# Optimization experiments

Measured on AMD Instinct MI355X. Metric: run time of the kernel, lower is better.

## Reference

```python
import jax, jax.numpy as jnp
import numpy as np

EPS = 1e-12


def sage_pool_conv(x, src, dst, W_pool, b_pool, W_self, W_neigh, b, num_nodes):
    """DGL SAGEConv with aggregator_type='pool':
    h_neigh[v] = max_{u in N(v)} relu(x[u] @ W_pool + b_pool)
    out[v] = x[v] @ W_self + h_neigh[v] @ W_neigh + b
    Zero-in-degree nodes get h_neigh = 0 (DGL fills max over empty set with 0).
    """
    m = jax.nn.relu(x[src] @ W_pool + b_pool)            # [E, F] gathered + transformed
    agg = jax.ops.segment_max(m, dst, num_segments=num_nodes)  # [N, F], -inf where no neighbors
    agg = jnp.where(jnp.isneginf(agg), 0.0, agg)
    return x @ W_self + agg @ W_neigh + b


def l2norm_relu(h):
    # F.normalize(h, p=2, dim=1, eps=1e-12) then relu
    n = jnp.maximum(jnp.linalg.norm(h, axis=1, keepdims=True), EPS)
    return jax.nn.relu(h / n)


def setup_inputs() -> dict:
    key = jax.random.key(0)
    N, E = 50000, 1600000
    IN, HID, OUT = 128, 128, 128
    ks = jax.random.split(key, 16)
    s = 0.05
    return {
        "x": jax.random.normal(ks[0], (N, IN), dtype=jnp.float32),
        "src": jax.random.randint(ks[1], (E,), 0, N, dtype=jnp.int32),
        "dst": jax.random.randint(ks[2], (E,), 0, N, dtype=jnp.int32),
        "W_pool1": jax.random.normal(ks[3], (IN, IN), dtype=jnp.float32) * s,
        "b_pool1": jnp.zeros((IN,), dtype=jnp.float32),
        "W_self1": jax.random.normal(ks[4], (IN, HID), dtype=jnp.float32) * s,
        "W_neigh1": jax.random.normal(ks[5], (IN, HID), dtype=jnp.float32) * s,
        "b1": jnp.zeros((HID,), dtype=jnp.float32),
        "W_pool2": jax.random.normal(ks[6], (HID, HID), dtype=jnp.float32) * s,
        "b_pool2": jnp.zeros((HID,), dtype=jnp.float32),
        "W_self2": jax.random.normal(ks[7], (HID, OUT), dtype=jnp.float32) * s,
        "W_neigh2": jax.random.normal(ks[8], (HID, OUT), dtype=jnp.float32) * s,
        "b2": jnp.zeros((OUT,), dtype=jnp.float32),
    }


def reference(x, src, dst, W_pool1, b_pool1, W_self1, W_neigh1, b1,
              W_pool2, b_pool2, W_self2, W_neigh2, b2):
    N = x.shape[0]
    h = sage_pool_conv(x, src, dst, W_pool1, b_pool1, W_self1, W_neigh1, b1, N)
    h = l2norm_relu(h)
    # dropout_1 is re-assigned in the original forward but never applied -> no dropout
    h = sage_pool_conv(h, src, dst, W_pool2, b_pool2, W_self2, W_neigh2, b2, N)
    h = l2norm_relu(h)
    return h
```

## Files before the change

### kernel.cpp

```cpp
#include <hip/hip_runtime.h>
#include <hip/hip_bf16.h>

#define NF 128

typedef __attribute__((ext_vector_type(8))) short bf8;
typedef __attribute__((ext_vector_type(4))) float f4;
typedef unsigned short u16x8 __attribute__((ext_vector_type(8)));

static __device__ __forceinline__ unsigned short f2bf(float f) {
  unsigned u = __builtin_bit_cast(unsigned, f);
  u = u + 0x7FFF + ((u >> 16) & 1);
  return (unsigned short)(u >> 16);
}

static __device__ __forceinline__ uint4 pkmax4(uint4 a, uint4 b) {
  u16x8 x = __builtin_bit_cast(u16x8, a);
  u16x8 y = __builtin_bit_cast(u16x8, b);
  u16x8 m = __builtin_elementwise_max(x, y);
  return __builtin_bit_cast(uint4, m);
}

static __device__ __forceinline__ uint4 shflxor4(uint4 a, int m) {
  uint4 r;
  r.x = (unsigned)__shfl_xor((int)a.x, m, 64);
  r.y = (unsigned)__shfl_xor((int)a.y, m, 64);
  r.z = (unsigned)__shfl_xor((int)a.z, m, 64);
  r.w = (unsigned)__shfl_xor((int)a.w, m, 64);
  return r;
}


__global__ void k_convX(const float* __restrict__ A, unsigned short* __restrict__ B,
                        long long nelem, int* __restrict__ bcnt, int nb) {
  long long i = (long long)(blockIdx.x * blockDim.x + threadIdx.x) * 8;
  if (blockIdx.x == 0 && (int)threadIdx.x < nb) bcnt[threadIdx.x] = 0;
  if (i + 8 > nelem) return;
  float4 a = *(const float4*)(A + i);
  float4 b = *(const float4*)(A + i + 4);
  uint4 o;
  o.x = f2bf(a.x) | ((unsigned)f2bf(a.y) << 16);
  o.y = f2bf(a.z) | ((unsigned)f2bf(a.w) << 16);
  o.z = f2bf(b.x) | ((unsigned)f2bf(b.y) << 16);
  o.w = f2bf(b.z) | ((unsigned)f2bf(b.w) << 16);
  *(uint4*)(B + i) = o;
}


__global__ void k_packW(const float* W0, const float* W1, const float* W2,
                        const float* W3, const float* W4, const float* W5,
                        unsigned short* __restrict__ out) {
  int gid = blockIdx.x * blockDim.x + threadIdx.x;
  int m = gid >> 11;
  int u = gid & 2047;
  if (m >= 6) return;
  const float* W = (m == 0) ? W0 : (m == 1) ? W1 : (m == 2) ? W2
                 : (m == 3) ? W3 : (m == 4) ? W4 : W5;
  int l = u & 63, c = u >> 6;
  int kk = c & 3, t = c >> 2;
  int kb = kk * 32 + ((l >> 4) << 3);
  int n = t * 16 + (l & 15);
  unsigned short* o = out + (size_t)m * 2048 * 8 + (size_t)u * 8;
  #pragma unroll
  for (int j = 0; j < 8; ++j) o[j] = f2bf(W[(size_t)(kb + j) * NF + n]);
}


#define TILE_B 8192

__global__ __launch_bounds__(256) void k_bhist(const int* __restrict__ dst,
                                               int* __restrict__ bcnt, int E) {
  __shared__ int h[256];
  int tid = threadIdx.x;
  h[tid] = 0;
  __syncthreads();
  int t0 = blockIdx.x * TILE_B;
  int tend = min(E, t0 + TILE_B);
  for (int i = t0 + tid; i < tend; i += 256) atomicAdd(&h[dst[i] >> 8], 1);
  __syncthreads();
  if (h[tid] > 0) atomicAdd(&bcnt[tid], h[tid]);
}

__global__ __launch_bounds__(256) void k_bscan(const int* __restrict__ bcnt,
                                               int* __restrict__ boff,
                                               int* __restrict__ cursors,
                                               int* __restrict__ off,
                                               int nb, int N, int E) {
  __shared__ int sc[256];
  int tid = threadIdx.x;
  int v = (tid < nb) ? bcnt[tid] : 0;
  sc[tid] = v;
  __syncthreads();
  for (int d = 1; d < 256; d <<= 1) {
    int t = (tid >= d) ? sc[tid - d] : 0;
    __syncthreads();
    sc[tid] += t;
    __syncthreads();
  }
  if (tid < nb) {
    boff[tid + 1] = sc[tid];
    cursors[tid] = sc[tid] - v;
  }
  if (tid == 0) { boff[0] = 0; off[N] = E; }
}

__global__ __launch_bounds__(256) void k_binB(const int* __restrict__ src,
                                              const int* __restrict__ dst,
                                              int* __restrict__ cursors,
                                              unsigned* __restrict__ tmp, int E) {
  __shared__ int h[256], sc[256], gb[256], lc[256];
  __shared__ unsigned sorted[TILE_B];
  int tid = threadIdx.x;
  int t0 = blockIdx.x * TILE_B;
  int tcnt = min(E - t0, TILE_B);
  if (tcnt <= 0) return;
  h[tid] = 0;
  __syncthreads();
  for (int i = tid; i < tcnt; i += 256) atomicAdd(&h[dst[t0 + i] >> 8], 1);
  __syncthreads();
  int v = h[tid];
  sc[tid] = v;
  __syncthreads();
  for (int d = 1; d < 256; d <<= 1) {
    int t = (tid >= d) ? sc[tid - d] : 0;
    __syncthreads();
    sc[tid] += t;
    __syncthreads();
  }
  lc[tid] = 0;
  gb[tid] = (v > 0) ? atomicAdd(&cursors[tid], v) : 0;
  __syncthreads();
  for (int i = tid; i < tcnt; i += 256) {
    int d = dst[t0 + i];
    unsigned s = (unsigned)src[t0 + i];
    int b = d >> 8;
    int p = (sc[b] - h[b]) + atomicAdd(&lc[b], 1);
    sorted[p] = ((unsigned)b << 24) | (s << 8) | (unsigned)(d & 255);
  }
  __syncthreads();
  for (int i = tid; i < tcnt; i += 256) {
    unsigned ev = sorted[i];
    int b = ev >> 24;
    tmp[gb[b] + (i - (sc[b] - h[b]))] = ev & 0xFFFFFFu;
  }
}

#define CSR_CAP 15360

__global__ __launch_bounds__(256) void k_binC(const unsigned* __restrict__ tmp,
                                              const int* __restrict__ boff,
                                              int* __restrict__ off,
                                              unsigned short* __restrict__ esrc, int N) {
  __shared__ int lh[256], ls[256], lcur[256];
  __shared__ int csr[CSR_CAP];
  int tid = threadIdx.x;
  int b = blockIdx.x;
  int base = b << 8;
  int beg = boff[b], end = boff[b + 1];
  int cnt = end - beg;
  lh[tid] = 0;
  __syncthreads();
  for (int i = beg + tid; i < end; i += 256) atomicAdd(&lh[tmp[i] & 255], 1);
  __syncthreads();
  int v = lh[tid];
  ls[tid] = v;
  __syncthreads();
  for (int d = 1; d < 256; d <<= 1) {
    int t = (tid >= d) ? ls[tid - d] : 0;
    __syncthreads();
    ls[tid] += t;
    __syncthreads();
  }
  int excl = ls[tid] - v;
  if (base + tid < N) off[base + tid] = beg + excl;
  lcur[tid] = 0;
  __syncthreads();
  if (cnt <= CSR_CAP) {
    for (int i = beg + tid; i < end; i += 256) {
      unsigned e = tmp[i];
      int dl = (int)(e & 255);
      int p = (ls[dl] - lh[dl]) + atomicAdd(&lcur[dl], 1);
      csr[p] = (int)(e >> 8);
    }
    __syncthreads();
    for (int i = tid; i < cnt; i += 256) esrc[beg + i] = (unsigned short)csr[i];
  } else {
    for (int i = beg + tid; i < end; i += 256) {
      unsigned e = tmp[i];
      int dl = (int)(e & 255);
      int p = (ls[dl] - lh[dl]) + atomicAdd(&lcur[dl], 1);
      esrc[beg + p] = (unsigned short)(e >> 8);
    }
  }
}


__global__ __launch_bounds__(256) void k_gemm_pool(
    const unsigned short* __restrict__ A, const unsigned short* __restrict__ P,
    const float* __restrict__ bias, unsigned short* __restrict__ Yout, int M) {
  __shared__ __align__(16) char smem[32768];
  int tid = threadIdx.x, w = tid >> 6, lane = tid & 63;
  int r0 = lane & 15, g = lane >> 4;
  int base = blockIdx.x * 64;
  int arow = min(base + w * 16 + r0, M - 1);

  {
    uint4* S = (uint4*)smem;
    const uint4* Pv = (const uint4*)P;
    for (int t = tid; t < 2048; t += 256) S[t] = Pv[t];
  }
  __syncthreads();

  f4 acc[8];
  #pragma unroll
  for (int t = 0; t < 8; ++t) acc[t] = (f4){0.f, 0.f, 0.f, 0.f};

  const bf8* Ar = (const bf8*)(A + (size_t)arow * NF);
  const bf8* Wl = (const bf8*)smem;
  #pragma unroll
  for (int kk = 0; kk < 4; ++kk) {
    bf8 a = Ar[kk * 4 + g];
    #pragma unroll
    for (int t = 0; t < 8; ++t) {
      bf8 b = Wl[(t * 4 + kk) * 64 + lane];
      acc[t] = __builtin_amdgcn_mfma_f32_16x16x32_bf16(a, b, acc[t], 0, 0, 0);
    }
  }

  float bb[8];
  #pragma unroll
  for (int t = 0; t < 8; ++t) bb[t] = bias[t * 16 + r0];

  __syncthreads();
  unsigned short* So = (unsigned short*)smem;
  #pragma unroll
  for (int i = 0; i < 4; ++i)
    #pragma unroll
    for (int t = 0; t < 8; ++t)
      So[(w * 16 + g * 4 + i) * NF + t * 16 + r0] = f2bf(fmaxf(acc[t][i] + bb[t], 0.f));
  __syncthreads();
  int maxrows = min(64, M - base);
  uint4* Og = (uint4*)(Yout + (size_t)base * NF);
  const uint4* Sv = (const uint4*)smem;
  int maxc = maxrows * 16;
  for (int c = tid; c < 1024; c += 256)
    if (c < maxc) Og[c] = Sv[c];
}


__global__ __launch_bounds__(256) void k_gather_max(
    const unsigned short* __restrict__ Y, const int* __restrict__ off,
    const unsigned short* __restrict__ esrc, unsigned short* __restrict__ AGG, int N) {
  int w = (blockIdx.x * 256 + threadIdx.x) >> 6;
  int lane = threadIdx.x & 63;
  if (w >= N) return;
  int r0 = lane & 15, g = lane >> 4;
  int s = __builtin_amdgcn_readfirstlane(off[w]);
  int e = __builtin_amdgcn_readfirstlane(off[w + 1]);
  uint4 am[4];
  #pragma unroll
  for (int j = 0; j < 4; ++j) am[j] = (uint4){0u, 0u, 0u, 0u};
  for (int b0 = s; b0 < e; b0 += 64) {
    int cnt = min(64, e - b0);
    int idxv = (int)esrc[b0 + min(lane, cnt - 1)];
    for (int i = 0; i < cnt; i += 16) {
      #pragma unroll
      for (int j = 0; j < 4; ++j) {
        int eo = min(i + j * 4 + g, cnt - 1);
        int u = __shfl(idxv, eo, 64);
        uint4 v = *((const uint4*)(Y + (size_t)u * NF) + r0);
        am[j] = pkmax4(am[j], v);
      }
    }
  }
  uint4 a01 = pkmax4(am[0], am[1]);
  uint4 a23 = pkmax4(am[2], am[3]);
  uint4 a = pkmax4(a01, a23);
  a = pkmax4(a, shflxor4(a, 16));
  a = pkmax4(a, shflxor4(a, 32));
  if (g == 0) *(uint4*)(AGG + (size_t)w * NF + r0 * 8) = a;
}


template <int OUT_MODE>
__global__ __launch_bounds__(256) void k_gemm_dual(
    const unsigned short* __restrict__ A0, const unsigned short* __restrict__ P0,
    const unsigned short* __restrict__ A1, const unsigned short* __restrict__ P1,
    const float* __restrict__ bias, void* __restrict__ Cout, int M) {
  __shared__ __align__(16) char smem[65536];
  int tid = threadIdx.x, w = tid >> 6, lane = tid & 63;
  int r0 = lane & 15, g = lane >> 4;
  int base = blockIdx.x * 64;
  int arow = min(base + w * 16 + r0, M - 1);

  {
    uint4* S = (uint4*)smem;
    const uint4* Pv0 = (const uint4*)P0;
    const uint4* Pv1 = (const uint4*)P1;
    for (int t = tid; t < 2048; t += 256) S[t] = Pv0[t];
    for (int t = tid; t < 2048; t += 256) S[2048 + t] = Pv1[t];
  }
  __syncthreads();

  f4 acc[8];
  #pragma unroll
  for (int t = 0; t < 8; ++t) acc[t] = (f4){0.f, 0.f, 0.f, 0.f};

  #pragma unroll
  for (int mat = 0; mat < 2; ++mat) {
    const unsigned short* A = (mat == 0) ? A0 : A1;
    const bf8* Ar = (const bf8*)(A + (size_t)arow * NF);
    const bf8* Wl = (const bf8*)smem + (size_t)mat * 2048;
    #pragma unroll
    for (int kk = 0; kk < 4; ++kk) {
      bf8 a = Ar[kk * 4 + g];
      #pragma unroll
      for (int t = 0; t < 8; ++t) {
        bf8 b = Wl[(t * 4 + kk) * 64 + lane];
        acc[t] = __builtin_amdgcn_mfma_f32_16x16x32_bf16(a, b, acc[t], 0, 0, 0);
      }
    }
  }

  float bb[8];
  #pragma unroll
  for (int t = 0; t < 8; ++t) bb[t] = bias[t * 16 + r0];

  float val[8][4];
  #pragma unroll
  for (int t = 0; t < 8; ++t)
    #pragma unroll
    for (int i = 0; i < 4; ++i) val[t][i] = acc[t][i] + bb[t];

  float ss[4] = {0.f, 0.f, 0.f, 0.f};
  #pragma unroll
  for (int i = 0; i < 4; ++i)
    #pragma unroll
    for (int t = 0; t < 8; ++t) ss[i] += val[t][i] * val[t][i];
  #pragma unroll
  for (int d = 1; d < 16; d <<= 1)
    #pragma unroll
    for (int i = 0; i < 4; ++i) ss[i] += __shfl_xor(ss[i], d, 64);
  float inv[4];
  #pragma unroll
  for (int i = 0; i < 4; ++i) inv[i] = 1.f / fmaxf(sqrtf(ss[i]), 1e-12f);

  __syncthreads();
  int maxrows = min(64, M - base);

  if (OUT_MODE == 2) {
    float* So = (float*)smem;
    #pragma unroll
    for (int i = 0; i < 4; ++i)
      #pragma unroll
      for (int t = 0; t < 8; ++t)
        So[(w * 16 + g * 4 + i) * NF + t * 16 + r0] = fmaxf(val[t][i] * inv[i], 0.f);
    __syncthreads();
    uint4* Og = (uint4*)((float*)Cout + (size_t)base * NF);
    const uint4* Sv = (const uint4*)smem;
    int maxc = maxrows * 32;
    for (int c = tid; c < 2048; c += 256)
      if (c < maxc) Og[c] = Sv[c];
  } else {
    unsigned short* So = (unsigned short*)smem;
    #pragma unroll
    for (int i = 0; i < 4; ++i)
      #pragma unroll
      for (int t = 0; t < 8; ++t)
        So[(w * 16 + g * 4 + i) * NF + t * 16 + r0] = f2bf(fmaxf(val[t][i] * inv[i], 0.f));
    __syncthreads();
    uint4* Og = (uint4*)((unsigned short*)Cout + (size_t)base * NF);
    const uint4* Sv = (const uint4*)smem;
    int maxc = maxrows * 16;
    for (int c = tid; c < 1024; c += 256)
      if (c < maxc) Og[c] = Sv[c];
  }
}


extern "C" void kernel_launch(void* const* d_in, const int* in_sizes, int n_in,
                              void* d_out, int out_size, void* d_ws, size_t ws_size,
                              hipStream_t stream) {
  const float* x   = (const float*)d_in[0];
  const int*   src = (const int*)d_in[1];
  const int*   dst = (const int*)d_in[2];
  const float* Wp1 = (const float*)d_in[3];
  const float* bp1 = (const float*)d_in[4];
  const float* Ws1 = (const float*)d_in[5];
  const float* Wn1 = (const float*)d_in[6];
  const float* b1  = (const float*)d_in[7];
  const float* Wp2 = (const float*)d_in[8];
  const float* bp2 = (const float*)d_in[9];
  const float* Ws2 = (const float*)d_in[10];
  const float* Wn2 = (const float*)d_in[11];
  const float* b2  = (const float*)d_in[12];
  float* out = (float*)d_out;

  const int N = in_sizes[0] / NF;
  const int E = in_sizes[1];
  const int NB = (N + 255) >> 8;

  char* ws = (char*)d_ws;
  auto carve = [&](size_t bytes) { char* p = ws; ws += (bytes + 255) & ~(size_t)255; return p; };
  unsigned short* Xb    = (unsigned short*)carve((size_t)N * NF * 2);
  unsigned short* Yb    = (unsigned short*)carve((size_t)N * NF * 2);
  unsigned short* AGGb  = (unsigned short*)carve((size_t)N * NF * 2);
  unsigned short* Hb    = (unsigned short*)carve((size_t)N * NF * 2);
  unsigned short* Wpack = (unsigned short*)carve((size_t)6 * NF * NF * 2);
  int* off     = (int*)carve((size_t)(N + 1) * 4);
  int* bcnt    = (int*)carve((size_t)NB * 4);
  int* boff    = (int*)carve((size_t)(NB + 1) * 4);
  int* cursors = (int*)carve((size_t)NB * 4);
  unsigned* tmp = (unsigned*)carve((size_t)E * 4);
  unsigned short* esrc = (unsigned short*)carve((size_t)E * 2);

  unsigned short* Pp1 = Wpack + 0 * NF * NF;
  unsigned short* Ps1 = Wpack + 1 * NF * NF;
  unsigned short* Pn1 = Wpack + 2 * NF * NF;
  unsigned short* Pp2 = Wpack + 3 * NF * NF;
  unsigned short* Ps2 = Wpack + 4 * NF * NF;
  unsigned short* Pn2 = Wpack + 5 * NF * NF;

  const long long nelX = (long long)N * NF;
  const int gConv = (int)((nelX / 8 + 255) / 256);
  const int gPack = (6 * 2048 + 255) / 256;
  const int gTile = (E + TILE_B - 1) / TILE_B;
  const int gG    = (N + 63) / 64;
  const int gRW   = (N + 3) / 4;

  k_convX<<<gConv, 256, 0, stream>>>(x, Xb, nelX, bcnt, NB);
  k_packW<<<gPack, 256, 0, stream>>>(Wp1, Ws1, Wn1, Wp2, Ws2, Wn2, Wpack);

  k_bhist<<<gTile, 256, 0, stream>>>(dst, bcnt, E);
  k_bscan<<<1, 256, 0, stream>>>(bcnt, boff, cursors, off, NB, N, E);
  k_binB<<<gTile, 256, 0, stream>>>(src, dst, cursors, tmp, E);
  k_binC<<<NB, 256, 0, stream>>>(tmp, boff, off, esrc, N);

  k_gemm_pool<<<gG, 256, 0, stream>>>(Xb, Pp1, bp1, Yb, N);
  k_gather_max<<<gRW, 256, 0, stream>>>(Yb, off, esrc, AGGb, N);
  k_gemm_dual<1><<<gG, 256, 0, stream>>>(Xb, Ps1, AGGb, Pn1, b1, Hb, N);

  k_gemm_pool<<<gG, 256, 0, stream>>>(Hb, Pp2, bp2, Yb, N);
  k_gather_max<<<gRW, 256, 0, stream>>>(Yb, off, esrc, AGGb, N);
  k_gemm_dual<2><<<gG, 256, 0, stream>>>(Hb, Ps2, AGGb, Pn2, b2, out, N);
}
```

Baseline: 296.0 us.

## Merge prep kernels, use persistent GEMM blocks, deepen gather loads

Folds the bf16 conversion of x, the weight packing and the destination histogram into one prep kernel, with a memset zeroing the bucket counts, so fewer kernels are launched. Replaces the per-64-row GEMM kernels with one persistent template that uses 512-thread blocks and a fixed grid. Each wave loops over 16-row tiles and stages its output in a private shared-memory area, so weight loads are amortized and block-wide barriers are avoided. The gather-max kernel now issues 8 independent row loads before reducing them, to keep more memory requests in flight at the cost of more registers.

```diff
diff --git a/kernel.cpp b/kernel.cpp
--- a/kernel.cpp
+++ b/kernel.cpp
@@ -30,55 +30,53 @@
 }
 
 
-__global__ void k_convX(const float* __restrict__ A, unsigned short* __restrict__ B,
-                        long long nelem, int* __restrict__ bcnt, int nb) {
-  long long i = (long long)(blockIdx.x * blockDim.x + threadIdx.x) * 8;
-  if (blockIdx.x == 0 && (int)threadIdx.x < nb) bcnt[threadIdx.x] = 0;
-  if (i + 8 > nelem) return;
-  float4 a = *(const float4*)(A + i);
-  float4 b = *(const float4*)(A + i + 4);
-  uint4 o;
-  o.x = f2bf(a.x) | ((unsigned)f2bf(a.y) << 16);
-  o.y = f2bf(a.z) | ((unsigned)f2bf(a.w) << 16);
-  o.z = f2bf(b.x) | ((unsigned)f2bf(b.y) << 16);
-  o.w = f2bf(b.z) | ((unsigned)f2bf(b.w) << 16);
-  *(uint4*)(B + i) = o;
-}
-
-
-__global__ void k_packW(const float* W0, const float* W1, const float* W2,
-                        const float* W3, const float* W4, const float* W5,
-                        unsigned short* __restrict__ out) {
-  int gid = blockIdx.x * blockDim.x + threadIdx.x;
-  int m = gid >> 11;
-  int u = gid & 2047;
-  if (m >= 6) return;
-  const float* W = (m == 0) ? W0 : (m == 1) ? W1 : (m == 2) ? W2
-                 : (m == 3) ? W3 : (m == 4) ? W4 : W5;
-  int l = u & 63, c = u >> 6;
-  int kk = c & 3, t = c >> 2;
-  int kb = kk * 32 + ((l >> 4) << 3);
-  int n = t * 16 + (l & 15);
-  unsigned short* o = out + (size_t)m * 2048 * 8 + (size_t)u * 8;
-  #pragma unroll
-  for (int j = 0; j < 8; ++j) o[j] = f2bf(W[(size_t)(kb + j) * NF + n]);
-}
-
-
 #define TILE_B 8192
 
-__global__ __launch_bounds__(256) void k_bhist(const int* __restrict__ dst,
-                                               int* __restrict__ bcnt, int E) {
+__global__ __launch_bounds__(256) void k_prep(
+    const float* __restrict__ x, unsigned short* __restrict__ Xb, long long nelX,
+    const int* __restrict__ dst, int* __restrict__ bcnt, int E, int gTile,
+    const float* W0, const float* W1, const float* W2,
+    const float* W3, const float* W4, const float* W5,
+    unsigned short* __restrict__ Wpack) {
   __shared__ int h[256];
-  int tid = threadIdx.x;
-  h[tid] = 0;
-  __syncthreads();
-  int t0 = blockIdx.x * TILE_B;
-  int tend = min(E, t0 + TILE_B);
-  for (int i = t0 + tid; i < tend; i += 256) atomicAdd(&h[dst[i] >> 8], 1);
-  __syncthreads();
-  if (h[tid] > 0) atomicAdd(&bcnt[tid], h[tid]);
-}
+  int b = blockIdx.x, tid = threadIdx.x;
+
+  long long i = ((long long)b * 256 + tid) * 8;
+  if (i + 8 <= nelX) {
+    float4 a = *(const float4*)(x + i);
+    float4 c = *(const float4*)(x + i + 4);
+    uint4 o;
+    o.x = f2bf(a.x) | ((unsigned)f2bf(a.y) << 16);
+    o.y = f2bf(a.z) | ((unsigned)f2bf(a.w) << 16);
+    o.z = f2bf(c.x) | ((unsigned)f2bf(c.y) << 16);
+    o.w = f2bf(c.z) | ((unsigned)f2bf(c.w) << 16);
+    *(uint4*)(Xb + i) = o;
+  }
+
+  if (b < gTile) {
+    h[tid] = 0;
+    __syncthreads();
+    int t0 = b * TILE_B;
+    int tend = min(E, t0 + TILE_B);
+    for (int k = t0 + tid; k < tend; k += 256) atomicAdd(&h[dst[k] >> 8], 1);
+    __syncthreads();
+    if (h[tid] > 0) atomicAdd(&bcnt[tid], h[tid]);
+  } else if (b < gTile + 48) {
+    int gid = (b - gTile) * 256 + tid;
+    int m = gid >> 11;
+    int u = gid & 2047;
+    const float* W = (m == 0) ? W0 : (m == 1) ? W1 : (m == 2) ? W2
+                   : (m == 3) ? W3 : (m == 4) ? W4 : W5;
+    int l = u & 63, c = u >> 6;
+    int kk = c & 3, t = c >> 2;
+    int kb = kk * 32 + ((l >> 4) << 3);
+    int n = t * 16 + (l & 15);
+    unsigned short* o = Wpack + (size_t)m * 2048 * 8 + (size_t)u * 8;
+    #pragma unroll
+    for (int j = 0; j < 8; ++j) o[j] = f2bf(W[(size_t)(kb + j) * NF + n]);
+  }
+}
+
 
 __global__ __launch_bounds__(256) void k_bscan(const int* __restrict__ bcnt,
                                                int* __restrict__ boff,
@@ -194,35 +192,23 @@
 }
 
 
-__global__ __launch_bounds__(256) void k_gemm_pool(
-    const unsigned short* __restrict__ A, const unsigned short* __restrict__ P,
-    const float* __restrict__ bias, unsigned short* __restrict__ Yout, int M) {
-  __shared__ __align__(16) char smem[32768];
+template <int NMAT, int OUT_MODE>
+__global__ __launch_bounds__(512) void k_gemm_p(
+    const unsigned short* __restrict__ A0, const unsigned short* __restrict__ P0,
+    const unsigned short* __restrict__ A1, const unsigned short* __restrict__ P1,
+    const float* __restrict__ bias, void* __restrict__ Cout, int M) {
+  constexpr int STG = (OUT_MODE == 2) ? 8192 : 4096;
+  __shared__ __align__(16) char smem[NMAT * 32768 + 8 * STG];
   int tid = threadIdx.x, w = tid >> 6, lane = tid & 63;
   int r0 = lane & 15, g = lane >> 4;
-  int base = blockIdx.x * 64;
-  int arow = min(base + w * 16 + r0, M - 1);
 
   {
     uint4* S = (uint4*)smem;
-    const uint4* Pv = (const uint4*)P;
-    for (int t = tid; t < 2048; t += 256) S[t] = Pv[t];
-  }
-  __syncthreads();
-
-  f4 acc[8];
-  #pragma unroll
-  for (int t = 0; t < 8; ++t) acc[t] = (f4){0.f, 0.f, 0.f, 0.f};
-
-  const bf8* Ar = (const bf8*)(A + (size_t)arow * NF);
-  const bf8* Wl = (const bf8*)smem;
-  #pragma unroll
-  for (int kk = 0; kk < 4; ++kk) {
-    bf8 a = Ar[kk * 4 + g];
-    #pragma unroll
-    for (int t = 0; t < 8; ++t) {
-      bf8 b = Wl[(t * 4 + kk) * 64 + lane];
-      acc[t] = __builtin_amdgcn_mfma_f32_16x16x32_bf16(a, b, acc[t], 0, 0, 0);
+    const uint4* Pv0 = (const uint4*)P0;
+    for (int t = tid; t < 2048; t += 512) S[t] = Pv0[t];
+    if (NMAT == 2) {
+      const uint4* Pv1 = (const uint4*)P1;
+      for (int t = tid; t < 2048; t += 512) S[2048 + t] = Pv1[t];
     }
   }
 
@@ -231,19 +217,89 @@
   for (int t = 0; t < 8; ++t) bb[t] = bias[t * 16 + r0];
 
   __syncthreads();
-  unsigned short* So = (unsigned short*)smem;
-  #pragma unroll
-  for (int i = 0; i < 4; ++i)
+  const bf8* Wl = (const bf8*)smem;
+  char* myst = smem + NMAT * 32768 + w * STG;
+
+  int T = (M + 15) >> 4;
+  int stride = gridDim.x * 8;
+  for (int t0i = blockIdx.x * 8 + w; t0i < T; t0i += stride) {
+    int rowbase = t0i * 16;
+    int arow = min(rowbase + r0, M - 1);
+
+    f4 acc[8];
+    #pragma unroll
+    for (int t = 0; t < 8; ++t) acc[t] = (f4){0.f, 0.f, 0.f, 0.f};
+
+    #pragma unroll
+    for (int mat = 0; mat < NMAT; ++mat) {
+      const unsigned short* A = (mat == 0) ? A0 : A1;
+      const bf8* Ar = (const bf8*)(A + (size_t)arow * NF);
+      const bf8* Wm = Wl + mat * 2048;
+      #pragma unroll
+      for (int kk = 0; kk < 4; ++kk) {
+        bf8 a = Ar[kk * 4 + g];
+        #pragma unroll
+        for (int t = 0; t < 8; ++t)
+          acc[t] = __builtin_amdgcn_mfma_f32_16x16x32_bf16(a, Wm[(t * 4 + kk) * 64 + lane], acc[t], 0, 0, 0);
+      }
+    }
+
+    float val[8][4];
     #pragma unroll
     for (int t = 0; t < 8; ++t)
-      So[(w * 16 + g * 4 + i) * NF + t * 16 + r0] = f2bf(fmaxf(acc[t][i] + bb[t], 0.f));
-  __syncthreads();
-  int maxrows = min(64, M - base);
-  uint4* Og = (uint4*)(Yout + (size_t)base * NF);
-  const uint4* Sv = (const uint4*)smem;
-  int maxc = maxrows * 16;
-  for (int c = tid; c < 1024; c += 256)
-    if (c < maxc) Og[c] = Sv[c];
+      #pragma unroll
+      for (int i = 0; i < 4; ++i) val[t][i] = acc[t][i] + bb[t];
+
+    float inv[4] = {1.f, 1.f, 1.f, 1.f};
+    if (OUT_MODE != 0) {
+      float ss[4] = {0.f, 0.f, 0.f, 0.f};
+      #pragma unroll
+      for (int i = 0; i < 4; ++i)
+        #pragma unroll
+        for (int t = 0; t < 8; ++t) ss[i] += val[t][i] * val[t][i];
+      #pragma unroll
+      for (int d = 1; d < 16; d <<= 1)
+        #pragma unroll
+        for (int i = 0; i < 4; ++i) ss[i] += __shfl_xor(ss[i], d, 64);
+      #pragma unroll
+      for (int i = 0; i < 4; ++i) inv[i] = 1.f / fmaxf(sqrtf(ss[i]), 1e-12f);
+    }
+
+    int maxrows = min(16, M - rowbase);
+    if (OUT_MODE == 2) {
+      float* So = (float*)myst;
+      #pragma unroll
+      for (int i = 0; i < 4; ++i)
+        #pragma unroll
+        for (int t = 0; t < 8; ++t)
+          So[(g * 4 + i) * NF + t * 16 + r0] = fmaxf(val[t][i] * inv[i], 0.f);
+      uint4* Og = (uint4*)((float*)Cout + (size_t)rowbase * NF);
+      const uint4* Sv = (const uint4*)myst;
+      int maxc = maxrows * 32;
+      #pragma unroll
+      for (int k = 0; k < 8; ++k) {
+        int c = lane + k * 64;
+        if (c < maxc) Og[c] = Sv[c];
+      }
+    } else {
+      unsigned short* So = (unsigned short*)myst;
+      #pragma unroll
+      for (int i = 0; i < 4; ++i)
+        #pragma unroll
+        for (int t = 0; t < 8; ++t)
+          So[(g * 4 + i) * NF + t * 16 + r0] =
+              f2bf(OUT_MODE == 0 ? fmaxf(val[t][i] + 0.f, 0.f) * 1.f
+                                 : fmaxf(val[t][i] * inv[i], 0.f));
+      uint4* Og = (uint4*)((unsigned short*)Cout + (size_t)rowbase * NF);
+      const uint4* Sv = (const uint4*)myst;
+      int maxc = maxrows * 16;
+      #pragma unroll
+      for (int k = 0; k < 4; ++k) {
+        int c = lane + k * 64;
+        if (c < maxc) Og[c] = Sv[c];
+      }
+    }
+  }
 }
 
 
@@ -256,124 +312,31 @@
   int r0 = lane & 15, g = lane >> 4;
   int s = __builtin_amdgcn_readfirstlane(off[w]);
   int e = __builtin_amdgcn_readfirstlane(off[w + 1]);
-  uint4 am[4];
+  uint4 am[8];
   #pragma unroll
-  for (int j = 0; j < 4; ++j) am[j] = (uint4){0u, 0u, 0u, 0u};
+  for (int j = 0; j < 8; ++j) am[j] = (uint4){0u, 0u, 0u, 0u};
   for (int b0 = s; b0 < e; b0 += 64) {
     int cnt = min(64, e - b0);
     int idxv = (int)esrc[b0 + min(lane, cnt - 1)];
-    for (int i = 0; i < cnt; i += 16) {
-      #pragma unroll
-      for (int j = 0; j < 4; ++j) {
+    for (int i = 0; i < cnt; i += 32) {
+      uint4 v[8];
+      #pragma unroll
+      for (int j = 0; j < 8; ++j) {
         int eo = min(i + j * 4 + g, cnt - 1);
         int u = __shfl(idxv, eo, 64);
-        uint4 v = *((const uint4*)(Y + (size_t)u * NF) + r0);
-        am[j] = pkmax4(am[j], v);
+        v[j] = *((const uint4*)(Y + (size_t)u * NF) + r0);
       }
-    }
-  }
-  uint4 a01 = pkmax4(am[0], am[1]);
-  uint4 a23 = pkmax4(am[2], am[3]);
-  uint4 a = pkmax4(a01, a23);
+      #pragma unroll
+      for (int j = 0; j < 8; ++j) am[j] = pkmax4(am[j], v[j]);
+    }
+  }
+  am[0] = pkmax4(am[0], am[1]); am[2] = pkmax4(am[2], am[3]);
+  am[4] = pkmax4(am[4], am[5]); am[6] = pkmax4(am[6], am[7]);
+  am[0] = pkmax4(am[0], am[2]); am[4] = pkmax4(am[4], am[6]);
+  uint4 a = pkmax4(am[0], am[4]);
   a = pkmax4(a, shflxor4(a, 16));
   a = pkmax4(a, shflxor4(a, 32));
   if (g == 0) *(uint4*)(AGG + (size_t)w * NF + r0 * 8) = a;
-}
-
-
-template <int OUT_MODE>
-__global__ __launch_bounds__(256) void k_gemm_dual(
-    const unsigned short* __restrict__ A0, const unsigned short* __restrict__ P0,
-    const unsigned short* __restrict__ A1, const unsigned short* __restrict__ P1,
-    const float* __restrict__ bias, void* __restrict__ Cout, int M) {
-  __shared__ __align__(16) char smem[65536];
-  int tid = threadIdx.x, w = tid >> 6, lane = tid & 63;
-  int r0 = lane & 15, g = lane >> 4;
-  int base = blockIdx.x * 64;
-  int arow = min(base + w * 16 + r0, M - 1);
-
-  {
-    uint4* S = (uint4*)smem;
-    const uint4* Pv0 = (const uint4*)P0;
-    const uint4* Pv1 = (const uint4*)P1;
-    for (int t = tid; t < 2048; t += 256) S[t] = Pv0[t];
-    for (int t = tid; t < 2048; t += 256) S[2048 + t] = Pv1[t];
-  }
-  __syncthreads();
-
-  f4 acc[8];
-  #pragma unroll
-  for (int t = 0; t < 8; ++t) acc[t] = (f4){0.f, 0.f, 0.f, 0.f};
-
-  #pragma unroll
-  for (int mat = 0; mat < 2; ++mat) {
-    const unsigned short* A = (mat == 0) ? A0 : A1;
-    const bf8* Ar = (const bf8*)(A + (size_t)arow * NF);
-    const bf8* Wl = (const bf8*)smem + (size_t)mat * 2048;
-    #pragma unroll
-    for (int kk = 0; kk < 4; ++kk) {
-      bf8 a = Ar[kk * 4 + g];
-      #pragma unroll
-      for (int t = 0; t < 8; ++t) {
-        bf8 b = Wl[(t * 4 + kk) * 64 + lane];
-        acc[t] = __builtin_amdgcn_mfma_f32_16x16x32_bf16(a, b, acc[t], 0, 0, 0);
-      }
-    }
-  }
-
-  float bb[8];
-  #pragma unroll
-  for (int t = 0; t < 8; ++t) bb[t] = bias[t * 16 + r0];
-
-  float val[8][4];
-  #pragma unroll
-  for (int t = 0; t < 8; ++t)
-    #pragma unroll
-    for (int i = 0; i < 4; ++i) val[t][i] = acc[t][i] + bb[t];
-
-  float ss[4] = {0.f, 0.f, 0.f, 0.f};
-  #pragma unroll
-  for (int i = 0; i < 4; ++i)
-    #pragma unroll
-    for (int t = 0; t < 8; ++t) ss[i] += val[t][i] * val[t][i];
-  #pragma unroll
-  for (int d = 1; d < 16; d <<= 1)
-    #pragma unroll
-    for (int i = 0; i < 4; ++i) ss[i] += __shfl_xor(ss[i], d, 64);
-  float inv[4];
-  #pragma unroll
-  for (int i = 0; i < 4; ++i) inv[i] = 1.f / fmaxf(sqrtf(ss[i]), 1e-12f);
-
-  __syncthreads();
-  int maxrows = min(64, M - base);
-
-  if (OUT_MODE == 2) {
-    float* So = (float*)smem;
-    #pragma unroll
-    for (int i = 0; i < 4; ++i)
-      #pragma unroll
-      for (int t = 0; t < 8; ++t)
-        So[(w * 16 + g * 4 + i) * NF + t * 16 + r0] = fmaxf(val[t][i] * inv[i], 0.f);
-    __syncthreads();
-    uint4* Og = (uint4*)((float*)Cout + (size_t)base * NF);
-    const uint4* Sv = (const uint4*)smem;
-    int maxc = maxrows * 32;
-    for (int c = tid; c < 2048; c += 256)
-      if (c < maxc) Og[c] = Sv[c];
-  } else {
-    unsigned short* So = (unsigned short*)smem;
-    #pragma unroll
-    for (int i = 0; i < 4; ++i)
-      #pragma unroll
-      for (int t = 0; t < 8; ++t)
-        So[(w * 16 + g * 4 + i) * NF + t * 16 + r0] = f2bf(fmaxf(val[t][i] * inv[i], 0.f));
-    __syncthreads();
-    uint4* Og = (uint4*)((unsigned short*)Cout + (size_t)base * NF);
-    const uint4* Sv = (const uint4*)smem;
-    int maxc = maxrows * 16;
-    for (int c = tid; c < 1024; c += 256)
-      if (c < maxc) Og[c] = Sv[c];
-  }
 }
 
 
@@ -422,24 +385,21 @@
 
   const long long nelX = (long long)N * NF;
   const int gConv = (int)((nelX / 8 + 255) / 256);
-  const int gPack = (6 * 2048 + 255) / 256;
   const int gTile = (E + TILE_B - 1) / TILE_B;
-  const int gG    = (N + 63) / 64;
   const int gRW   = (N + 3) / 4;
 
-  k_convX<<<gConv, 256, 0, stream>>>(x, Xb, nelX, bcnt, NB);
-  k_packW<<<gPack, 256, 0, stream>>>(Wp1, Ws1, Wn1, Wp2, Ws2, Wn2, Wpack);
-
-  k_bhist<<<gTile, 256, 0, stream>>>(dst, bcnt, E);
+  hipMemsetAsync(bcnt, 0, (size_t)NB * 4, stream);
+  k_prep<<<gConv, 256, 0, stream>>>(x, Xb, nelX, dst, bcnt, E, gTile,
+                                    Wp1, Ws1, Wn1, Wp2, Ws2, Wn2, Wpack);
   k_bscan<<<1, 256, 0, stream>>>(bcnt, boff, cursors, off, NB, N, E);
   k_binB<<<gTile, 256, 0, stream>>>(src, dst, cursors, tmp, E);
   k_binC<<<NB, 256, 0, stream>>>(tmp, boff, off, esrc, N);
 
-  k_gemm_pool<<<gG, 256, 0, stream>>>(Xb, Pp1, bp1, Yb, N);
+  k_gemm_p<1, 0><<<512, 512, 0, stream>>>(Xb, Pp1, nullptr, nullptr, bp1, Yb, N);
   k_gather_max<<<gRW, 256, 0, stream>>>(Yb, off, esrc, AGGb, N);
-  k_gemm_dual<1><<<gG, 256, 0, stream>>>(Xb, Ps1, AGGb, Pn1, b1, Hb, N);
-
-  k_gemm_pool<<<gG, 256, 0, stream>>>(Hb, Pp2, bp2, Yb, N);
+  k_gemm_p<2, 1><<<256, 512, 0, stream>>>(Xb, Ps1, AGGb, Pn1, b1, Hb, N);
+
+  k_gemm_p<1, 0><<<512, 512, 0, stream>>>(Hb, Pp2, nullptr, nullptr, bp2, Yb, N);
   k_gather_max<<<gRW, 256, 0, stream>>>(Yb, off, esrc, AGGb, N);
-  k_gemm_dual<2><<<gG, 256, 0, stream>>>(Hb, Ps2, AGGb, Pn2, b2, out, N);
-}
+  k_gemm_p<2, 2><<<256, 512, 0, stream>>>(Hb, Ps2, AGGb, Pn2, b2, out, N);
+}
```

Result: no change. 300.2 us (+1.4%).
